# Kernel tuning notes

Measured on AMD Instinct MI355X. Metric: run time of the kernel, lower is better.

## Reference

```python
import jax, jax.numpy as jnp
import numpy as np


def setup_inputs() -> dict:
    key = jax.random.key(0)
    k1, k2 = jax.random.split(key)
    x = jax.random.normal(k1, (16, 64, 256, 256), dtype=jnp.float32)
    haar = jax.random.normal(k2, (256, 256), dtype=jnp.float32)
    return {"x": x, "haar": haar}


def reference(x, haar):
    # x: [B, C, N, N]; haar: [N, N]
    B, C, N, _ = x.shape
    # (|x|+1)/(|x|+1) is exactly 1 with zero gradient; kept to mirror the
    # original graph's broadcast of the haar matrices against the input.
    ones = (jnp.abs(x) + 1.0) / (jnp.abs(x) + 1.0)
    # Per channel the looped batch_dots compute tmp[b,i,j]=sum_k A[k,i] X[b,j,k],
    # r[b,i,j]=sum_k tmp[b,k,i] A^T[j,k], which nets out to r = X @ A @ A.
    res = jnp.einsum('bcim,mk,kj->bcij', x * ones, haar, haar)
    # K.concatenate over channels along axis -1, then reshape (-1, C, N, N).
    # (This scrambles data across channel/row dims; replicate exactly.)
    cat = jnp.transpose(res, (0, 2, 1, 3)).reshape(B, N, C * N)
    out = cat.reshape(B, C, N, N)[:, :, : N // 2, : N // 2]
    return out
```

## Files before the change

kernel.cpp:

```cpp
#include <hip/hip_runtime.h>
#include <hip/hip_bf16.h>


typedef __attribute__((ext_vector_type(8))) short bf16x8;
typedef __attribute__((ext_vector_type(4))) float f32x4;

static __device__ inline unsigned short bf16bits(float f) {
    __hip_bfloat16 h = __float2bfloat16(f);
    return *reinterpret_cast<unsigned short*>(&h);
}

__global__ void h2swz_kernel(const float* __restrict__ haar,
                             unsigned short* __restrict__ bswz) {
    __shared__ float rowk[256];
    __shared__ float part[128];
    const int k   = blockIdx.x;
    const int tid = threadIdx.x;
    const int n   = tid & 127;
    const int h   = tid >> 7;
    rowk[tid] = haar[k * 256 + tid];
    __syncthreads();
    float acc = 0.f;
    const int t0 = h * 128;
#pragma unroll 8
    for (int t = 0; t < 128; ++t)
        acc = fmaf(rowk[t0 + t], haar[(t0 + t) * 256 + n], acc);
    if (h) part[n] = acc;
    __syncthreads();
    if (!h) {
        const int fb = n >> 4, lr = n & 15;
        const int s = k >> 5, lg = (k >> 3) & 3, e = k & 7;
        const size_t idx = ((((size_t)(fb * 8 + s)) * 64 + lg * 16 + lr) << 3) + e;
        bswz[idx] = bf16bits(acc + part[n]);
    }
}

__global__ __launch_bounds__(512, 2)
void wavelet_gemm_kernel(const float* __restrict__ x,
                         const uint4* __restrict__ bswz16,
                         float* __restrict__ out) {
    __shared__ __align__(16) char lds[131072];
    const int tid  = threadIdx.x;
    const int lane = tid & 63;
    const int w    = tid >> 6;
    const int lr   = lane & 15;
    const int lg   = lane >> 4;

    {
        uint4* bdst = reinterpret_cast<uint4*>(lds + 65536);
#pragma unroll
        for (int r = 0; r < 8; ++r)
            bdst[r * 512 + tid] = bswz16[r * 512 + tid];
    }

    f32x4 rv[16];
    const int mat0 = blockIdx.x * 4;
    {
        const float* xb = x + (size_t)mat0 * 65536;
#pragma unroll
        for (int q = 0; q < 16; ++q) {
            const int m = w * 16 + q;
            const int i = ((m >> 1) << 2) | (m & 1);
            rv[q] = reinterpret_cast<const f32x4*>(xb + i * 256)[lane];
        }
    }

    __syncthreads();

    for (int it = 0; it < 4; ++it) {
        const int blk = mat0 + it;
        const int c = blk & 63, b = blk >> 6;

#pragma unroll
        for (int q = 0; q < 16; ++q) {
            const int lm = w * 16 + q;
            union { unsigned short u[4]; unsigned long long d; } p;
            p.u[0] = bf16bits(rv[q].x);
            p.u[1] = bf16bits(rv[q].y);
            p.u[2] = bf16bits(rv[q].z);
            p.u[3] = bf16bits(rv[q].w);
            const int byte = (lm * 512 + lane * 8) ^ ((lm & 7) << 4);
            *reinterpret_cast<unsigned long long*>(lds + byte) = p.d;
        }

        if (it < 3) {
            const float* xb = x + (size_t)(blk + 1) * 65536;
#pragma unroll
            for (int q = 0; q < 16; ++q) {
                const int m = w * 16 + q;
                const int i = ((m >> 1) << 2) | (m & 1);
                rv[q] = reinterpret_cast<const f32x4*>(xb + i * 256)[lane];
            }
        }

        f32x4 acc[8] = {};
#pragma unroll
        for (int s = 0; s < 8; ++s) {
            const int lm = w * 16 + lr;
            const int abyte = (lm * 512 + s * 64 + lg * 16) ^ ((lm & 7) << 4);
            const bf16x8 aF = *reinterpret_cast<const bf16x8*>(lds + abyte);
#pragma unroll
            for (int fb = 0; fb < 8; ++fb) {
                const bf16x8 bF = *reinterpret_cast<const bf16x8*>(
                    lds + 65536 + (((fb * 8 + s) * 64 + lane) << 4));
                acc[fb] = __builtin_amdgcn_mfma_f32_16x16x32_bf16(aF, bF, acc[fb], 0, 0, 0);
            }
        }

#pragma unroll
        for (int fb = 0; fb < 8; ++fb) {
            const int j = fb * 16 + lr;
#pragma unroll
            for (int r = 0; r < 4; ++r) {
                const int m = w * 16 + lg * 4 + r;
                const size_t oidx =
                    (((size_t)b * 64 + (m >> 1)) * 128 + (m & 1) * 64 + c) * 128 + j;
                out[oidx] = acc[fb][r];
            }
        }
    }
}

extern "C" void kernel_launch(void* const* d_in, const int* in_sizes, int n_in,
                              void* d_out, int out_size, void* d_ws, size_t ws_size,
                              hipStream_t stream) {
    const float* x    = (const float*)d_in[0];
    const float* haar = (const float*)d_in[1];
    float* out = (float*)d_out;
    unsigned short* bswz = (unsigned short*)d_ws;

    h2swz_kernel<<<dim3(256), dim3(256), 0, stream>>>(haar, bswz);
    wavelet_gemm_kernel<<<dim3(256), dim3(512), 0, stream>>>(
        x, reinterpret_cast<const uint4*>(bswz), out);
}
```

Baseline: 46.27 us.

## Permute B columns for vectorized output stores and double-buffer input prefetch

The B-matrix swizzle is changed so each lane's eight MFMA output columns become two contiguous groups of four, which lets the epilogue issue 16-byte vector stores instead of scalar 4-byte stores. The input prefetch now uses two register buffers, loading matrix it+2 while it+1 is already resident, and the iteration loop is fully unrolled. The precompute kernel also splits its dot product across four accumulators for more ILP. Doubling the prefetch registers (128 extra VGPRs) risks spilling or losing occupancy under the 512x2 launch bound.

```diff
diff --git a/kernel.cpp b/kernel.cpp
--- a/kernel.cpp
+++ b/kernel.cpp
@@ -20,15 +20,21 @@
     const int h   = tid >> 7;
     rowk[tid] = haar[k * 256 + tid];
     __syncthreads();
-    float acc = 0.f;
+    float a0 = 0.f, a1 = 0.f, a2 = 0.f, a3 = 0.f;
     const int t0 = h * 128;
 #pragma unroll 8
-    for (int t = 0; t < 128; ++t)
-        acc = fmaf(rowk[t0 + t], haar[(t0 + t) * 256 + n], acc);
+    for (int t = 0; t < 128; t += 4) {
+        a0 = fmaf(rowk[t0 + t + 0], haar[(t0 + t + 0) * 256 + n], a0);
+        a1 = fmaf(rowk[t0 + t + 1], haar[(t0 + t + 1) * 256 + n], a1);
+        a2 = fmaf(rowk[t0 + t + 2], haar[(t0 + t + 2) * 256 + n], a2);
+        a3 = fmaf(rowk[t0 + t + 3], haar[(t0 + t + 3) * 256 + n], a3);
+    }
+    const float acc = (a0 + a1) + (a2 + a3);
     if (h) part[n] = acc;
     __syncthreads();
     if (!h) {
-        const int fb = n >> 4, lr = n & 15;
+        const int hi = n >> 6, lr = (n & 63) >> 2, q = n & 3;
+        const int fb = hi * 4 + q;
         const int s = k >> 5, lg = (k >> 3) & 3, e = k & 7;
         const size_t idx = ((((size_t)(fb * 8 + s)) * 64 + lg * 16 + lr) << 3) + e;
         bswz[idx] = bf16bits(acc + part[n]);
@@ -53,43 +59,49 @@
             bdst[r * 512 + tid] = bswz16[r * 512 + tid];
     }
 
-    f32x4 rv[16];
     const int mat0 = blockIdx.x * 4;
-    {
-        const float* xb = x + (size_t)mat0 * 65536;
+
+    f32x4 rvA[16], rvB[16];
 #pragma unroll
-        for (int q = 0; q < 16; ++q) {
-            const int m = w * 16 + q;
-            const int i = ((m >> 1) << 2) | (m & 1);
-            rv[q] = reinterpret_cast<const f32x4*>(xb + i * 256)[lane];
-        }
+    for (int q = 0; q < 16; ++q) {
+        const int m = w * 16 + q;
+        const int i = ((m >> 1) << 2) | (m & 1);
+        rvA[q] = reinterpret_cast<const f32x4*>(x + (size_t)mat0 * 65536 + i * 256)[lane];
+    }
+#pragma unroll
+    for (int q = 0; q < 16; ++q) {
+        const int m = w * 16 + q;
+        const int i = ((m >> 1) << 2) | (m & 1);
+        rvB[q] = reinterpret_cast<const f32x4*>(x + (size_t)(mat0 + 1) * 65536 + i * 256)[lane];
     }
 
     __syncthreads();
 
+#pragma unroll
     for (int it = 0; it < 4; ++it) {
         const int blk = mat0 + it;
         const int c = blk & 63, b = blk >> 6;
+        f32x4* cur = (it & 1) ? rvB : rvA;
 
 #pragma unroll
         for (int q = 0; q < 16; ++q) {
             const int lm = w * 16 + q;
             union { unsigned short u[4]; unsigned long long d; } p;
-            p.u[0] = bf16bits(rv[q].x);
-            p.u[1] = bf16bits(rv[q].y);
-            p.u[2] = bf16bits(rv[q].z);
-            p.u[3] = bf16bits(rv[q].w);
+            p.u[0] = bf16bits(cur[q].x);
+            p.u[1] = bf16bits(cur[q].y);
+            p.u[2] = bf16bits(cur[q].z);
+            p.u[3] = bf16bits(cur[q].w);
             const int byte = (lm * 512 + lane * 8) ^ ((lm & 7) << 4);
             *reinterpret_cast<unsigned long long*>(lds + byte) = p.d;
         }
 
-        if (it < 3) {
-            const float* xb = x + (size_t)(blk + 1) * 65536;
+        if (it < 2) {
+            const float* xb = x + (size_t)(blk + 2) * 65536;
 #pragma unroll
             for (int q = 0; q < 16; ++q) {
                 const int m = w * 16 + q;
                 const int i = ((m >> 1) << 2) | (m & 1);
-                rv[q] = reinterpret_cast<const f32x4*>(xb + i * 256)[lane];
+                cur[q] = reinterpret_cast<const f32x4*>(xb + i * 256)[lane];
             }
         }
 
@@ -108,15 +120,13 @@
         }
 
 #pragma unroll
-        for (int fb = 0; fb < 8; ++fb) {
-            const int j = fb * 16 + lr;
-#pragma unroll
-            for (int r = 0; r < 4; ++r) {
-                const int m = w * 16 + lg * 4 + r;
-                const size_t oidx =
-                    (((size_t)b * 64 + (m >> 1)) * 128 + (m & 1) * 64 + c) * 128 + j;
-                out[oidx] = acc[fb][r];
-            }
+        for (int r = 0; r < 4; ++r) {
+            const int m = w * 16 + lg * 4 + r;
+            float* rowp = out + (((size_t)b * 64 + (m >> 1)) * 128 + (m & 1) * 64 + c) * 128;
+            f32x4 v0 = {acc[0][r], acc[1][r], acc[2][r], acc[3][r]};
+            f32x4 v1 = {acc[4][r], acc[5][r], acc[6][r], acc[7][r]};
+            *reinterpret_cast<f32x4*>(rowp + lr * 4)      = v0;
+            *reinterpret_cast<f32x4*>(rowp + 64 + lr * 4) = v1;
         }
     }
 }
```

Result: faster. 45.17 us (-2.4%).
